# Optimization experiments

Hardware: AMD Instinct MI355X
Metric: run time of the kernel (lower is better)

The kernel has to match this reference:

```python
import jax, jax.numpy as jnp
import numpy as np

B, S, IN_F, OUT_F, R = 4, 4096, 4096, 4096, 1024  # new_r = sqrt((4096+4096)*128) = 1024


def setup_inputs() -> dict:
    key = jax.random.key(0)
    kx, kw, kb, ka = jax.random.split(key, 4)
    x = jax.random.normal(kx, (B, S, IN_F), dtype=jnp.float32)
    W = jax.random.normal(kw, (OUT_F, IN_F), dtype=jnp.float32) * 0.02
    b = jax.random.normal(kb, (OUT_F,), dtype=jnp.float32) * 0.02
    A = jax.random.normal(ka, (R, R), dtype=jnp.float32) * 0.02  # lora_A.weight (init zeros in module; randn here to exercise math)
    return {"x": x, "W": W, "b": b, "A": A}


def reference(x, W, b, A):
    # base linear: y = x @ W.T + b
    result = jnp.einsum('bsi,oi->bso', x, W) + b
    # MoRA adapter, mora_type=1, in_f % r == 0 (no padding needed)
    r = A.shape[0]
    sum_inter = IN_F // r  # 4
    in_x = x.reshape(*x.shape[:-1], sum_inter, r).sum(axis=-2)  # [B,S,r]
    out_x = jnp.einsum('bsr,qr->bsq', in_x, A)  # lora_A(in_x): in_x @ A.T
    repeat_time = -(-OUT_F // r)  # ceil = 4
    out_x = jnp.tile(out_x, (1, 1, repeat_time))[..., :OUT_F]
    return result + out_x
```

## Files before the change

### kernel.cpp

```cpp
#include <hip/hip_runtime.h>
#include <hip/hip_bf16.h>
#include <cstdint>


typedef __attribute__((ext_vector_type(8))) short bf16x8;
typedef __attribute__((ext_vector_type(16))) float f32x16;
typedef __attribute__((ext_vector_type(4))) float fvec4;

static constexpr int MTOT = 16384;
static constexpr int KF   = 4096;
static constexpr int NF   = 4096;
static constexpr int BM = 256, BN = 256, BK = 32;
static constexpr int TILE = BM * BK;
static constexpr int KT = KF / BK;
static constexpr int MB = MTOT / BM;
static constexpr int NB = NF / BN;

__global__ __launch_bounds__(256) void tile_x_kernel(const float* __restrict__ x,
                                                     __hip_bfloat16* __restrict__ xt) {
    int blk = blockIdx.x;
    int mb = blk >> 7, kt = blk & 127;
    int tid = threadIdx.x;
    __hip_bfloat16* dst = xt + (size_t)blk * TILE;
#pragma unroll
    for (int it = 0; it < 4; ++it) {
        int e = (it * 256 + tid) * 8;
        int f = e >> 9;
        int l = (e >> 3) & 63;
        int rb = f >> 1, kh = f & 1;
        int row = mb * BM + rb * 32 + (l & 31);
        int k0  = kt * BK + kh * 16 + (l >> 5) * 8;
        const fvec4* s = (const fvec4*)(x + (size_t)row * KF + k0);
        fvec4 v0 = s[0], v1 = s[1];
        union { bf16x8 v; __hip_bfloat16 h[8]; } o;
        o.h[0] = __float2bfloat16(v0[0]); o.h[1] = __float2bfloat16(v0[1]);
        o.h[2] = __float2bfloat16(v0[2]); o.h[3] = __float2bfloat16(v0[3]);
        o.h[4] = __float2bfloat16(v1[0]); o.h[5] = __float2bfloat16(v1[1]);
        o.h[6] = __float2bfloat16(v1[2]); o.h[7] = __float2bfloat16(v1[3]);
        *(bf16x8*)(dst + e) = o.v;
    }
}

__global__ __launch_bounds__(256) void tile_w_kernel(const float* __restrict__ W,
                                                     const float* __restrict__ A,
                                                     __hip_bfloat16* __restrict__ wt) {
    int blk = blockIdx.x;
    int nb = blk >> 7, kt = blk & 127;
    int tid = threadIdx.x;
    __hip_bfloat16* dst = wt + (size_t)blk * TILE;
#pragma unroll
    for (int it = 0; it < 4; ++it) {
        int e = (it * 256 + tid) * 8;
        int f = e >> 9;
        int l = (e >> 3) & 63;
        int rb = f >> 1, kh = f & 1;
        int o  = nb * BN + rb * 32 + (l & 31);
        int k0 = kt * BK + kh * 16 + (l >> 5) * 8;
        const fvec4* sw = (const fvec4*)(W + (size_t)o * KF + k0);
        const fvec4* sa = (const fvec4*)(A + (size_t)(o & 1023) * 1024 + (k0 & 1023));
        fvec4 w0 = sw[0], w1 = sw[1];
        fvec4 a0 = sa[0], a1 = sa[1];
        union { bf16x8 v; __hip_bfloat16 h[8]; } ov;
        ov.h[0] = __float2bfloat16(w0[0] + a0[0]); ov.h[1] = __float2bfloat16(w0[1] + a0[1]);
        ov.h[2] = __float2bfloat16(w0[2] + a0[2]); ov.h[3] = __float2bfloat16(w0[3] + a0[3]);
        ov.h[4] = __float2bfloat16(w1[0] + a1[0]); ov.h[5] = __float2bfloat16(w1[1] + a1[1]);
        ov.h[6] = __float2bfloat16(w1[2] + a1[2]); ov.h[7] = __float2bfloat16(w1[3] + a1[3]);
        *(bf16x8*)(dst + e) = ov.v;
    }
}

__device__ inline void gload_lds16(const __hip_bfloat16* g, __hip_bfloat16* l) {
    __builtin_amdgcn_global_load_lds(
        (const __attribute__((address_space(1))) unsigned int*)g,
        (__attribute__((address_space(3))) unsigned int*)l, 16, 0, 0);
}

#define STG(tt, sl) { const __hip_bfloat16* ga = aP + (size_t)(tt) * TILE;       \
    gload_lds16(ga, As + (sl) * TILE + t8);                                      \
    gload_lds16(ga + 4096, As + (sl) * TILE + 4096 + t8);                        \
    const __hip_bfloat16* gb = bP + (size_t)(tt) * TILE;                         \
    gload_lds16(gb, Bs + (sl) * TILE + t8);                                      \
    gload_lds16(gb + 4096, Bs + (sl) * TILE + 4096 + t8); }

#define PHASE(SL, STAGE_STMT) {                                                  \
    STAGE_STMT;                                                                  \
    bf16x8 af[8], bfv[4];                                                        \
    {                                                                            \
        const __hip_bfloat16* ab = As + (SL) * TILE + aOff;                      \
        af[0] = *(const bf16x8*)(ab);                                            \
        af[1] = *(const bf16x8*)(ab + 512);                                      \
        af[2] = *(const bf16x8*)(ab + 1024);                                     \
        af[3] = *(const bf16x8*)(ab + 1536);                                     \
        af[4] = *(const bf16x8*)(ab + 2048);                                     \
        af[5] = *(const bf16x8*)(ab + 2560);                                     \
        af[6] = *(const bf16x8*)(ab + 3072);                                     \
        af[7] = *(const bf16x8*)(ab + 3584);                                     \
        const __hip_bfloat16* bb = Bs + (SL) * TILE + bOff;                      \
        bfv[0] = *(const bf16x8*)(bb);                                           \
        bfv[1] = *(const bf16x8*)(bb + 512);                                     \
        bfv[2] = *(const bf16x8*)(bb + 1024);                                    \
        bfv[3] = *(const bf16x8*)(bb + 1536);                                    \
    }                                                                            \
    __builtin_amdgcn_s_setprio(1);                                               \
    _Pragma("unroll") for (int fm = 0; fm < 4; ++fm)                             \
        _Pragma("unroll") for (int fn = 0; fn < 2; ++fn) {                       \
            acc[fm][fn] = __builtin_amdgcn_mfma_f32_32x32x16_bf16(               \
                af[fm * 2 + 0], bfv[fn * 2 + 0], acc[fm][fn], 0, 0, 0);          \
            acc[fm][fn] = __builtin_amdgcn_mfma_f32_32x32x16_bf16(               \
                af[fm * 2 + 1], bfv[fn * 2 + 1], acc[fm][fn], 0, 0, 0);          \
        }                                                                        \
    __builtin_amdgcn_s_setprio(0);                                               \
    asm volatile("s_waitcnt vmcnt(8)" ::: "memory");                             \
    __builtin_amdgcn_s_barrier();                                                \
    asm volatile("" ::: "memory"); }

__global__ __launch_bounds__(512, 2) void gemm_bf16_kernel(
    const __hip_bfloat16* __restrict__ xt, const __hip_bfloat16* __restrict__ wt,
    const float* __restrict__ bias, float* __restrict__ out) {
    extern __shared__ __hip_bfloat16 lds[];
    __hip_bfloat16* As = lds;
    __hip_bfloat16* Bs = lds + 4 * TILE;

    int bid = blockIdx.x;
    int wg = (bid & 7) * 128 + (bid >> 3);
    int nb = wg >> 6;
    int mb = wg & 63;

    int tid = threadIdx.x;
    int lane = tid & 63;
    int wv = tid >> 6;
    int wm = wv >> 2, wn = wv & 3;
    int t8 = tid * 8;

    int aOff = wm * 4096 + lane * 8;
    int bOff = wn * 2048 + lane * 8;

    const __hip_bfloat16* aP = xt + (size_t)mb * (KT * TILE) + t8;
    const __hip_bfloat16* bP = wt + (size_t)nb * (KT * TILE) + t8;

    f32x16 acc[4][2];
#pragma unroll
    for (int fm = 0; fm < 4; ++fm)
#pragma unroll
        for (int fn = 0; fn < 2; ++fn)
#pragma unroll
            for (int r = 0; r < 16; ++r) acc[fm][fn][r] = 0.f;

    STG(0, 0); STG(1, 1); STG(2, 2);
    asm volatile("s_waitcnt vmcnt(8)" ::: "memory");
    __builtin_amdgcn_s_barrier();
    asm volatile("" ::: "memory");

    for (int j = 0; j < KT / 4; ++j) {
        int tb = 4 * j;
        int t4 = tb + 4; if (t4 >= KT) t4 = 0;
        int t5 = tb + 5; if (t5 >= KT) t5 = 0;
        int t6 = tb + 6; if (t6 >= KT) t6 = 0;
        PHASE(0, STG(tb + 3, 3));
        PHASE(1, STG(t4, 0));
        PHASE(2, STG(t5, 1));
        PHASE(3, STG(t6, 2));
    }
    asm volatile("s_waitcnt vmcnt(0)" ::: "memory");

    int row0 = mb * BM + wm * 128;
    int col0 = nb * BN + wn * 64;
    int ln31 = lane & 31;
    int l5 = lane >> 5;
#pragma unroll
    for (int fn = 0; fn < 2; ++fn) {
        int col = col0 + fn * 32 + ln31;
        float bv = bias[col];
#pragma unroll
        for (int fm = 0; fm < 4; ++fm) {
            int rbase = row0 + fm * 32 + 4 * l5;
#pragma unroll
            for (int r = 0; r < 16; ++r) {
                int row = rbase + (r & 3) + 8 * (r >> 2);
                out[(size_t)row * NF + col] = acc[fm][fn][r] + bv;
            }
        }
    }
}

extern "C" void kernel_launch(void* const* d_in, const int* in_sizes, int n_in,
                              void* d_out, int out_size, void* d_ws, size_t ws_size,
                              hipStream_t stream) {
    const float* x = (const float*)d_in[0];
    const float* W = (const float*)d_in[1];
    const float* b = (const float*)d_in[2];
    const float* A = (const float*)d_in[3];
    float* out = (float*)d_out;

    size_t xt_elems = (size_t)MB * KT * TILE;
    size_t wt_elems = (size_t)NB * KT * TILE;
    size_t need = (xt_elems + wt_elems) * sizeof(__hip_bfloat16);
    if (ws_size < need) return;

    __hip_bfloat16* xt = (__hip_bfloat16*)d_ws;
    __hip_bfloat16* wt = xt + xt_elems;

    (void)hipFuncSetAttribute((const void*)gemm_bf16_kernel,
                              hipFuncAttributeMaxDynamicSharedMemorySize, 131072);

    tile_x_kernel<<<MB * KT, 256, 0, stream>>>(x, xt);
    tile_w_kernel<<<NB * KT, 256, 0, stream>>>(W, A, wt);
    gemm_bf16_kernel<<<MB * NB, 512, 131072, stream>>>(xt, wt, b, out);
}
```

Baseline: 617.0 us.

## Software-pipeline LDS fragment reads across K-halves and tighten vmcnt wait

Each 32-wide K tile is split into two 16-wide halves with ping-pong register sets. The LDS reads for the next half, including the first half of the next tile, are issued before the MFMAs of the current half so LDS latency overlaps matrix math. The global-load wait is tightened from vmcnt(8) to vmcnt(4) so the next stage is resident before its early read. This aims to hide ds_read latency, at the cost of extra live registers and a shorter prefetch slack on global loads.

```diff
diff --git a/kernel.cpp b/kernel.cpp
--- a/kernel.cpp
+++ b/kernel.cpp
@@ -82,35 +82,35 @@
     gload_lds16(gb, Bs + (sl) * TILE + t8);                                      \
     gload_lds16(gb + 4096, Bs + (sl) * TILE + 4096 + t8); }
 
-#define PHASE(SL, STAGE_STMT) {                                                  \
+#define RD_KH(P, SL, KH) {                                                       \
+    const __hip_bfloat16* ab_ = As + (SL) * TILE + aOff + (KH) * 512;            \
+    P##a0 = *(const bf16x8*)(ab_);                                               \
+    P##a1 = *(const bf16x8*)(ab_ + 1024);                                        \
+    P##a2 = *(const bf16x8*)(ab_ + 2048);                                        \
+    P##a3 = *(const bf16x8*)(ab_ + 3072);                                        \
+    const __hip_bfloat16* bb_ = Bs + (SL) * TILE + bOff + (KH) * 512;            \
+    P##b0 = *(const bf16x8*)(bb_);                                               \
+    P##b1 = *(const bf16x8*)(bb_ + 1024); }
+
+#define MM_KH(P) {                                                               \
+    __builtin_amdgcn_s_setprio(1);                                               \
+    acc[0][0] = __builtin_amdgcn_mfma_f32_32x32x16_bf16(P##a0, P##b0, acc[0][0], 0, 0, 0); \
+    acc[0][1] = __builtin_amdgcn_mfma_f32_32x32x16_bf16(P##a0, P##b1, acc[0][1], 0, 0, 0); \
+    acc[1][0] = __builtin_amdgcn_mfma_f32_32x32x16_bf16(P##a1, P##b0, acc[1][0], 0, 0, 0); \
+    acc[1][1] = __builtin_amdgcn_mfma_f32_32x32x16_bf16(P##a1, P##b1, acc[1][1], 0, 0, 0); \
+    acc[2][0] = __builtin_amdgcn_mfma_f32_32x32x16_bf16(P##a2, P##b0, acc[2][0], 0, 0, 0); \
+    acc[2][1] = __builtin_amdgcn_mfma_f32_32x32x16_bf16(P##a2, P##b1, acc[2][1], 0, 0, 0); \
+    acc[3][0] = __builtin_amdgcn_mfma_f32_32x32x16_bf16(P##a3, P##b0, acc[3][0], 0, 0, 0); \
+    acc[3][1] = __builtin_amdgcn_mfma_f32_32x32x16_bf16(P##a3, P##b1, acc[3][1], 0, 0, 0); \
+    __builtin_amdgcn_s_setprio(0); }
+
+#define TILE_STEP(SLT, SLN, STAGE_STMT) {                                        \
     STAGE_STMT;                                                                  \
-    bf16x8 af[8], bfv[4];                                                        \
-    {                                                                            \
-        const __hip_bfloat16* ab = As + (SL) * TILE + aOff;                      \
-        af[0] = *(const bf16x8*)(ab);                                            \
-        af[1] = *(const bf16x8*)(ab + 512);                                      \
-        af[2] = *(const bf16x8*)(ab + 1024);                                     \
-        af[3] = *(const bf16x8*)(ab + 1536);                                     \
-        af[4] = *(const bf16x8*)(ab + 2048);                                     \
-        af[5] = *(const bf16x8*)(ab + 2560);                                     \
-        af[6] = *(const bf16x8*)(ab + 3072);                                     \
-        af[7] = *(const bf16x8*)(ab + 3584);                                     \
-        const __hip_bfloat16* bb = Bs + (SL) * TILE + bOff;                      \
-        bfv[0] = *(const bf16x8*)(bb);                                           \
-        bfv[1] = *(const bf16x8*)(bb + 512);                                     \
-        bfv[2] = *(const bf16x8*)(bb + 1024);                                    \
-        bfv[3] = *(const bf16x8*)(bb + 1536);                                    \
-    }                                                                            \
-    __builtin_amdgcn_s_setprio(1);                                               \
-    _Pragma("unroll") for (int fm = 0; fm < 4; ++fm)                             \
-        _Pragma("unroll") for (int fn = 0; fn < 2; ++fn) {                       \
-            acc[fm][fn] = __builtin_amdgcn_mfma_f32_32x32x16_bf16(               \
-                af[fm * 2 + 0], bfv[fn * 2 + 0], acc[fm][fn], 0, 0, 0);          \
-            acc[fm][fn] = __builtin_amdgcn_mfma_f32_32x32x16_bf16(               \
-                af[fm * 2 + 1], bfv[fn * 2 + 1], acc[fm][fn], 0, 0, 0);          \
-        }                                                                        \
-    __builtin_amdgcn_s_setprio(0);                                               \
-    asm volatile("s_waitcnt vmcnt(8)" ::: "memory");                             \
+    RD_KH(B, SLT, 1)                                          \
+    MM_KH(A)                                                  \
+    RD_KH(A, SLN, 0)                                          \
+    MM_KH(B)                                                  \
+    asm volatile("s_waitcnt vmcnt(4)" ::: "memory");                             \
     __builtin_amdgcn_s_barrier();                                                \
     asm volatile("" ::: "memory"); }
 
@@ -146,20 +146,24 @@
 #pragma unroll
             for (int r = 0; r < 16; ++r) acc[fm][fn][r] = 0.f;
 
+    bf16x8 Aa0, Aa1, Aa2, Aa3, Ab0, Ab1;
+    bf16x8 Ba0, Ba1, Ba2, Ba3, Bb0, Bb1;
+
     STG(0, 0); STG(1, 1); STG(2, 2);
-    asm volatile("s_waitcnt vmcnt(8)" ::: "memory");
+    asm volatile("s_waitcnt vmcnt(4)" ::: "memory");
     __builtin_amdgcn_s_barrier();
     asm volatile("" ::: "memory");
+    RD_KH(A, 0, 0)
 
     for (int j = 0; j < KT / 4; ++j) {
         int tb = 4 * j;
         int t4 = tb + 4; if (t4 >= KT) t4 = 0;
         int t5 = tb + 5; if (t5 >= KT) t5 = 0;
         int t6 = tb + 6; if (t6 >= KT) t6 = 0;
-        PHASE(0, STG(tb + 3, 3));
-        PHASE(1, STG(t4, 0));
-        PHASE(2, STG(t5, 1));
-        PHASE(3, STG(t6, 2));
+        TILE_STEP(0, 1, STG(tb + 3, 3));
+        TILE_STEP(1, 2, STG(t4, 0));
+        TILE_STEP(2, 3, STG(t5, 1));
+        TILE_STEP(3, 0, STG(t6, 2));
     }
     asm volatile("s_waitcnt vmcnt(0)" ::: "memory");
 
```

Measured after the change: 615.2 us. No clear change (-0.3%).
